# Performance work log

Measured on AMD Instinct MI355X. Metric: run time of the kernel, lower is better.

Reference implementation:

```python
import jax, jax.numpy as jnp
import numpy as np

B, N, C, H = 16, 577, 384, 6
ONE_DIM = 24
RPD = 2 * ONE_DIM - 1  # 47
NUM_CLS = 1
HEAD_DIM = C // H
SCALE = HEAD_DIM ** -0.5


def _build_rel_pos_index():
    # Faithful to the torch loop: tmp[dy - y + off, dx - x + off] with
    # torch's negative-index wraparound -> modulo RPD.
    off = ONE_DIM // 2
    qy = np.repeat(np.arange(ONE_DIM), ONE_DIM)  # (Np,) y of each query patch
    qx = np.tile(np.arange(ONE_DIM), ONE_DIM)    # (Np,) x of each query patch
    ky, kx = qy, qx                              # key patches use same grid
    ry = (ky[None, :] - qy[:, None] + off) % RPD
    rx = (kx[None, :] - qx[:, None] + off) % RPD
    return jnp.asarray(ry * RPD + rx, dtype=jnp.int32)  # (Np, Np)


def setup_inputs() -> dict:
    key = jax.random.key(0)
    k = jax.random.split(key, 6)
    x = jax.random.normal(k[0], (B, N, C), dtype=jnp.float32)
    qkv_w = jax.random.normal(k[1], (3 * C, C), dtype=jnp.float32) * 0.02
    qkv_b = jnp.zeros((3 * C,), dtype=jnp.float32)
    proj_w = jax.random.normal(k[2], (C, C), dtype=jnp.float32) * 0.02
    proj_b = jnp.zeros((C,), dtype=jnp.float32)
    rel_pos = jax.random.normal(k[3], (H, RPD * RPD), dtype=jnp.float32) * 0.02
    mask = jax.random.randint(k[4], (B, N, N), 0, 2, dtype=jnp.int32)
    return {
        "x": x, "qkv_w": qkv_w, "qkv_b": qkv_b,
        "proj_w": proj_w, "proj_b": proj_b, "rel_pos": rel_pos,
        "rel_pos_index": _build_rel_pos_index(),
        "mask": mask, "patch_attn": 1,
    }


def reference(x, qkv_w, qkv_b, proj_w, proj_b, rel_pos, rel_pos_index, mask, patch_attn):
    # qkv projection: torch Linear -> x @ W^T + b
    qkv = x @ qkv_w.T + qkv_b                               # (B, N, 3C)
    qkv = qkv.reshape(B, N, 3, H, HEAD_DIM).transpose(2, 0, 3, 1, 4)
    q, k, v = qkv[0], qkv[1], qkv[2]                        # (B, H, N, hd)

    attn = jnp.einsum("bhqd,bhkd->bhqk", q, k) * SCALE      # (B, H, N, N)

    if patch_attn:
        # gather per-head relative-position bias for patch tokens
        bias = rel_pos[:, rel_pos_index]                    # (H, Np, Np)
        attn = attn.at[:, :, NUM_CLS:, NUM_CLS:].add(bias)

    neg = jnp.finfo(attn.dtype).min
    attn = jnp.where(mask[:, None, :, :] == 0, neg, attn)   # broadcast over heads

    attn = jax.nn.softmax(attn, axis=-1)
    out = jnp.einsum("bhqk,bhkd->bhqd", attn, v)            # (B, H, N, hd)
    out = out.transpose(0, 2, 1, 3).reshape(B, N, C)
    out = out @ proj_w.T + proj_b
    return out
```

## Files before the change

kernel.cpp:

```cpp
#include <hip/hip_runtime.h>
#include <float.h>
#include <math.h>

#define NB 16
#define NN 577
#define NC 384
#define NH 6
#define ND 64
#define RPD2 2209
#define MTOT 9232
#define MPAD 9344
#define SCALE_ 0.125f
#define NEGBIG -3.0e38f
#define BSTRIDE 580
#define NKPAD 640

typedef __attribute__((ext_vector_type(8))) short bf16x8;
typedef __attribute__((ext_vector_type(4))) float f32x4;
typedef unsigned short u16;

#define MFMA16(a, b, c) __builtin_amdgcn_mfma_f32_16x16x32_bf16(a, b, c, 0, 0, 0)

#define SQA 3932160ull
#define OFF_QH 0ull
#define OFF_QL SQA
#define OFF_KH (2ull * SQA)
#define OFF_KL (3ull * SQA)
#define OFF_VTH (4ull * SQA)
#define OFF_VTL (5ull * SQA)
#define OFF_XH (6ull * SQA)
#define OFF_XL (6ull * SQA + 3588096ull)
#define OFF_WQH (6ull * SQA + 2ull * 3588096ull)
#define OFF_WQL (OFF_WQH + 442368ull)
#define OFF_WPH (OFF_WQL + 442368ull)
#define OFF_WPL (OFF_WPH + 147456ull)
#define OFF_BT  (OFF_WPL + 147456ull)
#define OFF_PM  (OFF_BT + 2007960ull)

static __device__ __forceinline__ u16 f2bf(float f) {
  unsigned u = __float_as_uint(f);
  u += 0x7fff + ((u >> 16) & 1);
  return (u16)(u >> 16);
}
static __device__ __forceinline__ float bf2f(u16 h) {
  return __uint_as_float((unsigned)h << 16);
}
static __device__ __forceinline__ void split2(float v, u16& hi, u16& lo) {
  hi = f2bf(v);
  lo = f2bf(v - bf2f(hi));
}
static __device__ __forceinline__ void gload16(const void* g, void* l) {
  __builtin_amdgcn_global_load_lds(
      (const __attribute__((address_space(1))) void*)g,
      (__attribute__((address_space(3))) void*)l, 16, 0, 0);
}

__global__ __launch_bounds__(256) void split_inputs_k(
    const float* __restrict__ x, const float* __restrict__ wq,
    const float* __restrict__ wp, u16* __restrict__ ws)
{
  const int q = blockIdx.x * 256 + threadIdx.x;
  float4 v = {0.f, 0.f, 0.f, 0.f};
  u16 *dh, *dl;
  if (q < 897024) {
    if (q < 886272) v = ((const float4*)x)[q];
    dh = ws + OFF_XH + 4ull * q;
    dl = ws + OFF_XL + 4ull * q;
  } else if (q < 1007616) {
    int t = q - 897024;
    v = ((const float4*)wq)[t];
    dh = ws + OFF_WQH + 4ull * t;
    dl = ws + OFF_WQL + 4ull * t;
  } else {
    int t = q - 1007616;
    v = ((const float4*)wp)[t];
    dh = ws + OFF_WPH + 4ull * t;
    dl = ws + OFF_WPL + 4ull * t;
  }
  ushort4 hh, ll;
  split2(v.x, hh.x, ll.x);
  split2(v.y, hh.y, ll.y);
  split2(v.z, hh.z, ll.z);
  split2(v.w, hh.w, ll.w);
  *(ushort4*)dh = hh;
  *(ushort4*)dl = ll;
}

__global__ __launch_bounds__(256) void pack_mask_k(const int* __restrict__ mask,
                                                   unsigned* __restrict__ pm)
{
  const int wid = (blockIdx.x * 256 + threadIdx.x) >> 6;
  const int lane = threadIdx.x & 63;
  if (wid >= MTOT) return;
  const int* mr = mask + (size_t)wid * NN;
#pragma unroll
  for (int c = 0; c < 10; ++c) {
    int k = c * 64 + lane;
    int v = (k < NN) ? mr[k] : 0;
    unsigned long long bal = __ballot(v != 0);
    if (lane == 0) pm[wid * 20 + 2 * c] = (unsigned)bal;
    if (lane == 1) pm[wid * 20 + 2 * c + 1] = (unsigned)(bal >> 32);
  }
}

__global__ __launch_bounds__(256) void bias_build_k(
    const float* __restrict__ rel_pos, const int* __restrict__ rel_idx,
    const int* __restrict__ patch, u16* __restrict__ tbl)
{
  const int q = blockIdx.x;
  const int h = blockIdx.y;
  const int pa = *patch;
  u16* row = tbl + ((size_t)h * NN + q) * BSTRIDE;
  for (int kk = threadIdx.x; kk < BSTRIDE; kk += 256) {
    float v = 0.f;
    if (pa && q >= 1 && kk >= 1 && kk < NN)
      v = rel_pos[h * RPD2 + rel_idx[(q - 1) * 576 + (kk - 1)]];
    row[kk] = f2bf(v);
  }
}

__global__ __launch_bounds__(256, 3) void qkv_mfma_k(
    const u16* __restrict__ Xh, const u16* __restrict__ Xl,
    const u16* __restrict__ Wh, const u16* __restrict__ Wl,
    const float* __restrict__ bias, u16* __restrict__ ws)
{
  __shared__ u16 Ash[4096], Asl[4096];
  __shared__ u16 Bsh[4096], Bsl[4096];

  const int tid = threadIdx.x;
  const int w = tid >> 6, l = tid & 63, lq = l & 15, lg = l >> 4;
  const int wm = (w >> 1) * 64, wn = (w & 1) * 64;
  const int mb = blockIdx.x * 128;
  const int rb = blockIdx.y * 128;
  const int r0 = rb + wn;
  const int soff = (l >> 2) * 384 + (l & 3) * 8;

  f32x4 acc[4][4];
#pragma unroll
  for (int nt = 0; nt < 4; ++nt) {
    float bv = bias[r0 + 16 * nt + lq];
#pragma unroll
    for (int mt = 0; mt < 4; ++mt) acc[mt][nt] = (f32x4){bv, bv, bv, bv};
  }

  for (int k0 = 0; k0 < 384; k0 += 32) {
    __syncthreads();
#pragma unroll
    for (int j = 0; j < 2; ++j) {
      const int tr = 32 * w + 16 * j;
      const size_t ga = (size_t)(mb + tr) * 384 + k0 + soff;
      const size_t gb = (size_t)(rb + tr) * 384 + k0 + soff;
      gload16(&Xh[ga], &Ash[tr * 32]);
      gload16(&Xl[ga], &Asl[tr * 32]);
      gload16(&Wh[gb], &Bsh[tr * 32]);
      gload16(&Wl[gb], &Bsl[tr * 32]);
    }
    __syncthreads();

    bf16x8 bhf[4], blf[4];
#pragma unroll
    for (int nt = 0; nt < 4; ++nt) {
      bhf[nt] = *(const bf16x8*)&Bsh[(wn + 16 * nt + lq) * 32 + 8 * lg];
      blf[nt] = *(const bf16x8*)&Bsl[(wn + 16 * nt + lq) * 32 + 8 * lg];
    }
#pragma unroll
    for (int mt = 0; mt < 4; ++mt) {
      bf16x8 ah = *(const bf16x8*)&Ash[(wm + 16 * mt + lq) * 32 + 8 * lg];
      bf16x8 al = *(const bf16x8*)&Asl[(wm + 16 * mt + lq) * 32 + 8 * lg];
#pragma unroll
      for (int nt = 0; nt < 4; ++nt) {
        acc[mt][nt] = MFMA16(ah, bhf[nt], acc[mt][nt]);
        acc[mt][nt] = MFMA16(ah, blf[nt], acc[mt][nt]);
        acc[mt][nt] = MFMA16(al, bhf[nt], acc[mt][nt]);
      }
    }
  }

  const int comp = rb / 384;
  const int h = ((rb % 384) + wn) >> 6;
#pragma unroll
  for (int mt = 0; mt < 4; ++mt)
#pragma unroll
    for (int r = 0; r < 4; ++r) {
      int m = mb + wm + 16 * mt + 4 * lg + r;
      if (m >= MTOT) continue;
      int bb = m / NN, nn = m - bb * NN;
      int bh = bb * NH + h;
#pragma unroll
      for (int nt = 0; nt < 4; ++nt) {
        int d = 16 * nt + lq;
        float v = acc[mt][nt][r];
        u16 hi, lo;
        if (comp == 0) {
          v *= SCALE_;
          split2(v, hi, lo);
          size_t a = ((size_t)bh * NKPAD + nn) * 64 + d;
          ws[OFF_QH + a] = hi;
          ws[OFF_QL + a] = lo;
        } else if (comp == 1) {
          split2(v, hi, lo);
          size_t a = ((size_t)bh * NKPAD + nn) * 64 + d;
          ws[OFF_KH + a] = hi;
          ws[OFF_KL + a] = lo;
        } else {
          split2(v, hi, lo);
          size_t a = ((size_t)bh * 64 + d) * NKPAD + nn;
          ws[OFF_VTH + a] = hi;
          ws[OFF_VTL + a] = lo;
        }
      }
    }
}

__global__ __launch_bounds__(256, 3) void attn_k(
    const u16* __restrict__ Qh, const u16* __restrict__ Ql,
    const u16* __restrict__ Kh, const u16* __restrict__ Kl,
    const u16* __restrict__ Vth, const u16* __restrict__ Vtl,
    const u16* __restrict__ btbl, const unsigned* __restrict__ pm,
    u16* __restrict__ Oh, u16* __restrict__ Ol)
{
  __shared__ u16 Kth[4096], Ktl[4096];
  __shared__ u16 Vsh[4096], Vsl[4096];
  __shared__ u16 Ph[4][1024], Pl[4][1024];

  const int tid = threadIdx.x;
  const int w = tid >> 6, l = tid & 63, lq = l & 15, lg = l >> 4;
  const int q0 = blockIdx.x * 64;
  const int h = blockIdx.y, b = blockIdx.z;
  const int bh = b * NH + h;
  const int qrow = q0 + 16 * w + lq;
  const int swz = (lq & 7) << 3;
  const int ln8 = l >> 3, lc8 = l & 7;
  const int koff = ln8 * 64 + ((lc8 ^ ln8) << 3);
  const int voff = ln8 * NKPAD + ((lc8 ^ ln8) << 3);

  const size_t qbase = ((size_t)bh * NKPAD + qrow) * 64 + 8 * lg;
  bf16x8 qbh[2], qbl[2];
  qbh[0] = *(const bf16x8*)&Qh[qbase];
  qbh[1] = *(const bf16x8*)&Qh[qbase + 32];
  qbl[0] = *(const bf16x8*)&Ql[qbase];
  qbl[1] = *(const bf16x8*)&Ql[qbase + 32];

  const bool qv = qrow < NN;
  const int gqc = qv ? qrow : NN - 1;
  const unsigned* pmrow = pm + ((size_t)b * NN + gqc) * 20;
  const size_t brow = ((size_t)h * NN + gqc) * BSTRIDE;

  float m_reg = NEGBIG, l_reg = 0.f;
  f32x4 accO[4] = {};

  for (int ch = 0; ch < 10; ++ch) {
    const int kb = ch * 64;
    __syncthreads();
    {
      const size_t kgb = ((size_t)bh * NKPAD + kb + 16 * w) * 64 + koff;
      const size_t vgb = ((size_t)bh * 64 + 16 * w) * NKPAD + kb + voff;
      gload16(&Kh[kgb],                 &Kth[(16 * w) * 64]);
      gload16(&Kh[kgb + 512],           &Kth[(16 * w + 8) * 64]);
      gload16(&Kl[kgb],                 &Ktl[(16 * w) * 64]);
      gload16(&Kl[kgb + 512],           &Ktl[(16 * w + 8) * 64]);
      gload16(&Vth[vgb],                &Vsh[(16 * w) * 64]);
      gload16(&Vth[vgb + 8 * NKPAD],    &Vsh[(16 * w + 8) * 64]);
      gload16(&Vtl[vgb],                &Vsl[(16 * w) * 64]);
      gload16(&Vtl[vgb + 8 * NKPAD],    &Vsl[(16 * w + 8) * 64]);
    }
    unsigned long long m64 = (unsigned long long)pmrow[2 * ch] |
                             ((unsigned long long)pmrow[2 * ch + 1] << 32);
    f32x4 cinit[4];
#pragma unroll
    for (int t = 0; t < 4; ++t) {
      cinit[t] = (f32x4){0.f, 0.f, 0.f, 0.f};
      int kkb = kb + 16 * t + 4 * lg;
      if (qv && kkb <= 576) {
        ushort4 b4 = *(const ushort4*)&btbl[brow + kkb];
        cinit[t][0] = bf2f(b4.x); cinit[t][1] = bf2f(b4.y);
        cinit[t][2] = bf2f(b4.z); cinit[t][3] = bf2f(b4.w);
      }
    }
    __syncthreads();

    float sv[4][4];
#pragma unroll
    for (int t = 0; t < 4; ++t) {
      f32x4 acc = cinit[t];
      const int ar = (16 * t + lq) * 64;
#pragma unroll
      for (int ks = 0; ks < 2; ++ks) {
        const int c = (8 * lg + 32 * ks) ^ swz;
        bf16x8 ah = *(const bf16x8*)&Kth[ar + c];
        bf16x8 al = *(const bf16x8*)&Ktl[ar + c];
        acc = MFMA16(ah, qbh[ks], acc);
        acc = MFMA16(ah, qbl[ks], acc);
        acc = MFMA16(al, qbh[ks], acc);
      }
      sv[t][0] = acc[0]; sv[t][1] = acc[1];
      sv[t][2] = acc[2]; sv[t][3] = acc[3];
    }

    float cmax = NEGBIG;
#pragma unroll
    for (int t = 0; t < 4; ++t)
#pragma unroll
      for (int r = 0; r < 4; ++r) {
        int kl = 16 * t + 4 * lg + r;
        float s = ((m64 >> kl) & 1ull) ? sv[t][r] : NEGBIG;
        sv[t][r] = s;
        cmax = fmaxf(cmax, s);
      }
    cmax = fmaxf(cmax, __shfl_xor(cmax, 16));
    cmax = fmaxf(cmax, __shfl_xor(cmax, 32));
    float m_new = fmaxf(m_reg, cmax);
    float fx = __expf(m_reg - m_new);
    float csum = 0.f;
    float ev[4][4];
#pragma unroll
    for (int t = 0; t < 4; ++t)
#pragma unroll
      for (int r = 0; r < 4; ++r) {
        float e = __expf(sv[t][r] - m_new);
        ev[t][r] = e;
        csum += e;
      }
    csum += __shfl_xor(csum, 16);
    csum += __shfl_xor(csum, 32);
    l_reg = l_reg * fx + csum;
    m_reg = m_new;

#pragma unroll
    for (int t = 0; t < 4; ++t) {
      ushort4 ph, plo;
      split2(ev[t][0], ph.x, plo.x);
      split2(ev[t][1], ph.y, plo.y);
      split2(ev[t][2], ph.z, plo.z);
      split2(ev[t][3], ph.w, plo.w);
      int c = (16 * t + 4 * lg) ^ swz;
      *(ushort4*)&Ph[w][lq * 64 + c] = ph;
      *(ushort4*)&Pl[w][lq * 64 + c] = plo;
    }

    float fxr[4];
#pragma unroll
    for (int r = 0; r < 4; ++r) fxr[r] = __shfl(fx, 4 * lg + r);
#pragma unroll
    for (int t = 0; t < 4; ++t) {
      accO[t][0] *= fxr[0]; accO[t][1] *= fxr[1];
      accO[t][2] *= fxr[2]; accO[t][3] *= fxr[3];
    }

    bf16x8 pah[2], pal[2];
#pragma unroll
    for (int ks = 0; ks < 2; ++ks) {
      int c = (8 * lg + 32 * ks) ^ swz;
      pah[ks] = *(const bf16x8*)&Ph[w][lq * 64 + c];
      pal[ks] = *(const bf16x8*)&Pl[w][lq * 64 + c];
    }

#pragma unroll
    for (int t = 0; t < 4; ++t) {
      const int vr = (16 * t + lq) * 64;
#pragma unroll
      for (int ks = 0; ks < 2; ++ks) {
        const int c = (8 * lg + 32 * ks) ^ swz;
        bf16x8 vh = *(const bf16x8*)&Vsh[vr + c];
        bf16x8 vl = *(const bf16x8*)&Vsl[vr + c];
        accO[t] = MFMA16(pah[ks], vh, accO[t]);
        accO[t] = MFMA16(pal[ks], vh, accO[t]);
        accO[t] = MFMA16(pah[ks], vl, accO[t]);
      }
    }
  }

  float il = 1.f / l_reg;
  float ilr[4];
#pragma unroll
  for (int r = 0; r < 4; ++r) ilr[r] = __shfl(il, 4 * lg + r);
#pragma unroll
  for (int t = 0; t < 4; ++t)
#pragma unroll
    for (int r = 0; r < 4; ++r) {
      int gq2 = q0 + 16 * w + 4 * lg + r;
      if (gq2 < NN) {
        float v = accO[t][r] * ilr[r];
        u16 hi, lo;
        split2(v, hi, lo);
        size_t a = ((size_t)b * NN + gq2) * NC + h * 64 + 16 * t + lq;
        Oh[a] = hi;
        Ol[a] = lo;
      }
    }
}

__global__ __launch_bounds__(256, 3) void proj_mfma_k(
    const u16* __restrict__ Ah, const u16* __restrict__ Al,
    const u16* __restrict__ Wh, const u16* __restrict__ Wl,
    const float* __restrict__ bias, float* __restrict__ out)
{
  __shared__ u16 Ash[4096], Asl[4096];
  __shared__ u16 Bsh[4096], Bsl[4096];

  const int tid = threadIdx.x;
  const int w = tid >> 6, l = tid & 63, lq = l & 15, lg = l >> 4;
  const int wm = (w >> 1) * 64, wn = (w & 1) * 64;
  const int mb = blockIdx.x * 128;
  const int rb = blockIdx.y * 128;
  const int r0 = rb + wn;
  const int soff = (l >> 2) * 384 + (l & 3) * 8;

  f32x4 acc[4][4];
#pragma unroll
  for (int nt = 0; nt < 4; ++nt) {
    float bv = bias[r0 + 16 * nt + lq];
#pragma unroll
    for (int mt = 0; mt < 4; ++mt) acc[mt][nt] = (f32x4){bv, bv, bv, bv};
  }

  for (int k0 = 0; k0 < 384; k0 += 32) {
    __syncthreads();
#pragma unroll
    for (int j = 0; j < 2; ++j) {
      const int tr = 32 * w + 16 * j;
      const size_t ga = (size_t)(mb + tr) * 384 + k0 + soff;
      const size_t gb = (size_t)(rb + tr) * 384 + k0 + soff;
      gload16(&Ah[ga], &Ash[tr * 32]);
      gload16(&Al[ga], &Asl[tr * 32]);
      gload16(&Wh[gb], &Bsh[tr * 32]);
      gload16(&Wl[gb], &Bsl[tr * 32]);
    }
    __syncthreads();

    bf16x8 bhf[4], blf[4];
#pragma unroll
    for (int nt = 0; nt < 4; ++nt) {
      bhf[nt] = *(const bf16x8*)&Bsh[(wn + 16 * nt + lq) * 32 + 8 * lg];
      blf[nt] = *(const bf16x8*)&Bsl[(wn + 16 * nt + lq) * 32 + 8 * lg];
    }
#pragma unroll
    for (int mt = 0; mt < 4; ++mt) {
      bf16x8 ah = *(const bf16x8*)&Ash[(wm + 16 * mt + lq) * 32 + 8 * lg];
      bf16x8 al = *(const bf16x8*)&Asl[(wm + 16 * mt + lq) * 32 + 8 * lg];
#pragma unroll
      for (int nt = 0; nt < 4; ++nt) {
        acc[mt][nt] = MFMA16(ah, bhf[nt], acc[mt][nt]);
        acc[mt][nt] = MFMA16(ah, blf[nt], acc[mt][nt]);
        acc[mt][nt] = MFMA16(al, bhf[nt], acc[mt][nt]);
      }
    }
  }

#pragma unroll
  for (int mt = 0; mt < 4; ++mt)
#pragma unroll
    for (int r = 0; r < 4; ++r) {
      int m = mb + wm + 16 * mt + 4 * lg + r;
      if (m >= MTOT) continue;
#pragma unroll
      for (int nt = 0; nt < 4; ++nt)
        out[(size_t)m * NC + r0 + 16 * nt + lq] = acc[mt][nt][r];
    }
}

extern "C" void kernel_launch(void* const* d_in, const int* in_sizes, int n_in,
                              void* d_out, int out_size, void* d_ws, size_t ws_size,
                              hipStream_t stream) {
  const float* x       = (const float*)d_in[0];
  const float* qkv_w   = (const float*)d_in[1];
  const float* qkv_b   = (const float*)d_in[2];
  const float* proj_w  = (const float*)d_in[3];
  const float* proj_b  = (const float*)d_in[4];
  const float* rel_pos = (const float*)d_in[5];
  const int*   rel_idx = (const int*)d_in[6];
  const int*   mask    = (const int*)d_in[7];
  const int*   patch   = (const int*)d_in[8];
  float* out = (float*)d_out;
  u16* W16 = (u16*)d_ws;

  unsigned* pmp = (unsigned*)(W16 + OFF_PM);
  u16* btblp = W16 + OFF_BT;

  split_inputs_k<<<4080, 256, 0, stream>>>(x, qkv_w, proj_w, W16);
  pack_mask_k<<<2308, 256, 0, stream>>>(mask, pmp);
  bias_build_k<<<dim3(NN, NH), 256, 0, stream>>>(rel_pos, rel_idx, patch, btblp);
  qkv_mfma_k<<<dim3(73, 9), 256, 0, stream>>>(
      W16 + OFF_XH, W16 + OFF_XL, W16 + OFF_WQH, W16 + OFF_WQL, qkv_b, W16);
  attn_k<<<dim3(10, NH, NB), 256, 0, stream>>>(
      W16 + OFF_QH, W16 + OFF_QL, W16 + OFF_KH, W16 + OFF_KL,
      W16 + OFF_VTH, W16 + OFF_VTL, btblp, pmp,
      W16 + OFF_XH, W16 + OFF_XL);
  proj_mfma_k<<<dim3(73, 3), 256, 0, stream>>>(
      W16 + OFF_XH, W16 + OFF_XL, W16 + OFF_WPH, W16 + OFF_WPL, proj_b, out);
}
```

Measured before the change: 181.5 us.

## Rewrite attention kernel with 32x32 MFMA, 128-query tiles and XCD-aware block mapping

Switches the attention kernel from 16x16x32 to 32x32x16 bf16 MFMA, with each wave owning 32 query rows so a block covers 128 queries. K/V LDS tiles are reused across twice as many queries, halving block count and global K/V traffic. The P matrix is now kept as a single bf16 (dropping the lo term in PV, 2 MFMAs instead of 3), which reduces work but lowers precision of the softmax weights. Blocks are remapped so the same (b,h) lands on the same XCD for L2 locality.

```diff
diff --git a/kernel.cpp b/kernel.cpp
--- a/kernel.cpp
+++ b/kernel.cpp
@@ -17,9 +17,11 @@
 
 typedef __attribute__((ext_vector_type(8))) short bf16x8;
 typedef __attribute__((ext_vector_type(4))) float f32x4;
+typedef __attribute__((ext_vector_type(16))) float f32x16;
 typedef unsigned short u16;
 
 #define MFMA16(a, b, c) __builtin_amdgcn_mfma_f32_16x16x32_bf16(a, b, c, 0, 0, 0)
+#define MFMA32(a, b, c) __builtin_amdgcn_mfma_f32_32x32x16_bf16(a, b, c, 0, 0, 0)
 
 #define SQA 3932160ull
 #define OFF_QH 0ull
@@ -221,33 +223,39 @@
 {
   __shared__ u16 Kth[4096], Ktl[4096];
   __shared__ u16 Vsh[4096], Vsl[4096];
-  __shared__ u16 Ph[4][1024], Pl[4][1024];
+  __shared__ u16 Ps[4][2048];
 
   const int tid = threadIdx.x;
-  const int w = tid >> 6, l = tid & 63, lq = l & 15, lg = l >> 4;
-  const int q0 = blockIdx.x * 64;
-  const int h = blockIdx.y, b = blockIdx.z;
-  const int bh = b * NH + h;
-  const int qrow = q0 + 16 * w + lq;
-  const int swz = (lq & 7) << 3;
+  const int w = tid >> 6, l = tid & 63;
+  const int qc = l & 31, hi = l >> 5;
+
+  const int wg = blockIdx.x;
+  const int xcd = wg & 7, slot = wg >> 3;
+  const int bh = (slot / 5) * 8 + xcd;
+  const int qb = slot % 5;
+  const int b = bh / NH, h = bh % NH;
+  const int q0 = qb * 128;
+
+  const int q = q0 + 32 * w + qc;
   const int ln8 = l >> 3, lc8 = l & 7;
   const int koff = ln8 * 64 + ((lc8 ^ ln8) << 3);
   const int voff = ln8 * NKPAD + ((lc8 ^ ln8) << 3);
 
-  const size_t qbase = ((size_t)bh * NKPAD + qrow) * 64 + 8 * lg;
-  bf16x8 qbh[2], qbl[2];
-  qbh[0] = *(const bf16x8*)&Qh[qbase];
-  qbh[1] = *(const bf16x8*)&Qh[qbase + 32];
-  qbl[0] = *(const bf16x8*)&Ql[qbase];
-  qbl[1] = *(const bf16x8*)&Ql[qbase + 32];
-
-  const bool qv = qrow < NN;
-  const int gqc = qv ? qrow : NN - 1;
-  const unsigned* pmrow = pm + ((size_t)b * NN + gqc) * 20;
-  const size_t brow = ((size_t)h * NN + gqc) * BSTRIDE;
+  const size_t qrow = ((size_t)bh * NKPAD + q) * 64 + 8 * hi;
+  bf16x8 qfh[4], qfl[4];
+#pragma unroll
+  for (int st = 0; st < 4; ++st) {
+    qfh[st] = *(const bf16x8*)&Qh[qrow + 16 * st];
+    qfl[st] = *(const bf16x8*)&Ql[qrow + 16 * st];
+  }
+
+  const bool qv = q < NN;
+  const int gq = qv ? q : NN - 1;
+  const unsigned* pmrow = pm + ((size_t)b * NN + gq) * 20;
+  const size_t brow = ((size_t)h * NN + gq) * BSTRIDE;
 
   float m_reg = NEGBIG, l_reg = 0.f;
-  f32x4 accO[4] = {};
+  f32x16 accO[2] = {};
 
   for (int ch = 0; ch < 10; ++ch) {
     const int kb = ch * 64;
@@ -255,137 +263,131 @@
     {
       const size_t kgb = ((size_t)bh * NKPAD + kb + 16 * w) * 64 + koff;
       const size_t vgb = ((size_t)bh * 64 + 16 * w) * NKPAD + kb + voff;
-      gload16(&Kh[kgb],                 &Kth[(16 * w) * 64]);
-      gload16(&Kh[kgb + 512],           &Kth[(16 * w + 8) * 64]);
-      gload16(&Kl[kgb],                 &Ktl[(16 * w) * 64]);
-      gload16(&Kl[kgb + 512],           &Ktl[(16 * w + 8) * 64]);
-      gload16(&Vth[vgb],                &Vsh[(16 * w) * 64]);
-      gload16(&Vth[vgb + 8 * NKPAD],    &Vsh[(16 * w + 8) * 64]);
-      gload16(&Vtl[vgb],                &Vsl[(16 * w) * 64]);
-      gload16(&Vtl[vgb + 8 * NKPAD],    &Vsl[(16 * w + 8) * 64]);
+      gload16(&Kh[kgb],              &Kth[(16 * w) * 64]);
+      gload16(&Kh[kgb + 512],        &Kth[(16 * w + 8) * 64]);
+      gload16(&Kl[kgb],              &Ktl[(16 * w) * 64]);
+      gload16(&Kl[kgb + 512],        &Ktl[(16 * w + 8) * 64]);
+      gload16(&Vth[vgb],             &Vsh[(16 * w) * 64]);
+      gload16(&Vth[vgb + 8 * NKPAD], &Vsh[(16 * w + 8) * 64]);
+      gload16(&Vtl[vgb],             &Vsl[(16 * w) * 64]);
+      gload16(&Vtl[vgb + 8 * NKPAD], &Vsl[(16 * w + 8) * 64]);
     }
     unsigned long long m64 = (unsigned long long)pmrow[2 * ch] |
                              ((unsigned long long)pmrow[2 * ch + 1] << 32);
-    f32x4 cinit[4];
-#pragma unroll
-    for (int t = 0; t < 4; ++t) {
-      cinit[t] = (f32x4){0.f, 0.f, 0.f, 0.f};
-      int kkb = kb + 16 * t + 4 * lg;
-      if (qv && kkb <= 576) {
-        ushort4 b4 = *(const ushort4*)&btbl[brow + kkb];
-        cinit[t][0] = bf2f(b4.x); cinit[t][1] = bf2f(b4.y);
-        cinit[t][2] = bf2f(b4.z); cinit[t][3] = bf2f(b4.w);
-      }
-    }
-    __syncthreads();
-
-    float sv[4][4];
-#pragma unroll
-    for (int t = 0; t < 4; ++t) {
-      f32x4 acc = cinit[t];
-      const int ar = (16 * t + lq) * 64;
-#pragma unroll
-      for (int ks = 0; ks < 2; ++ks) {
-        const int c = (8 * lg + 32 * ks) ^ swz;
-        bf16x8 ah = *(const bf16x8*)&Kth[ar + c];
-        bf16x8 al = *(const bf16x8*)&Ktl[ar + c];
-        acc = MFMA16(ah, qbh[ks], acc);
-        acc = MFMA16(ah, qbl[ks], acc);
-        acc = MFMA16(al, qbh[ks], acc);
-      }
-      sv[t][0] = acc[0]; sv[t][1] = acc[1];
-      sv[t][2] = acc[2]; sv[t][3] = acc[3];
+    f32x16 s[2];
+#pragma unroll
+    for (int kt = 0; kt < 2; ++kt) {
+#pragma unroll
+      for (int m = 0; m < 4; ++m) {
+        int kkb = kb + 32 * kt + 8 * m + 4 * hi;
+        ushort4 b4 = {0, 0, 0, 0};
+        if (qv && kkb <= 576) b4 = *(const ushort4*)&btbl[brow + kkb];
+        s[kt][4 * m + 0] = bf2f(b4.x);
+        s[kt][4 * m + 1] = bf2f(b4.y);
+        s[kt][4 * m + 2] = bf2f(b4.z);
+        s[kt][4 * m + 3] = bf2f(b4.w);
+      }
+    }
+    __syncthreads();
+
+#pragma unroll
+    for (int kt = 0; kt < 2; ++kt) {
+      const int key = 32 * kt + qc;
+      const int rbase = key * 64;
+      const int sw = (key & 7);
+#pragma unroll
+      for (int st = 0; st < 4; ++st) {
+        const int addr = rbase + (((2 * st + hi) ^ sw) << 3);
+        bf16x8 ah = *(const bf16x8*)&Kth[addr];
+        bf16x8 al = *(const bf16x8*)&Ktl[addr];
+        s[kt] = MFMA32(ah, qfh[st], s[kt]);
+        s[kt] = MFMA32(ah, qfl[st], s[kt]);
+        s[kt] = MFMA32(al, qfh[st], s[kt]);
+      }
     }
 
     float cmax = NEGBIG;
 #pragma unroll
-    for (int t = 0; t < 4; ++t)
-#pragma unroll
-      for (int r = 0; r < 4; ++r) {
-        int kl = 16 * t + 4 * lg + r;
-        float s = ((m64 >> kl) & 1ull) ? sv[t][r] : NEGBIG;
-        sv[t][r] = s;
-        cmax = fmaxf(cmax, s);
-      }
-    cmax = fmaxf(cmax, __shfl_xor(cmax, 16));
+    for (int kt = 0; kt < 2; ++kt)
+#pragma unroll
+      for (int r = 0; r < 16; ++r) {
+        int bit = 32 * kt + (r & 3) + 8 * (r >> 2) + 4 * hi;
+        float v = ((m64 >> bit) & 1ull) ? s[kt][r] : NEGBIG;
+        s[kt][r] = v;
+        cmax = fmaxf(cmax, v);
+      }
     cmax = fmaxf(cmax, __shfl_xor(cmax, 32));
     float m_new = fmaxf(m_reg, cmax);
     float fx = __expf(m_reg - m_new);
     float csum = 0.f;
-    float ev[4][4];
-#pragma unroll
-    for (int t = 0; t < 4; ++t)
-#pragma unroll
-      for (int r = 0; r < 4; ++r) {
-        float e = __expf(sv[t][r] - m_new);
-        ev[t][r] = e;
-        csum += e;
-      }
-    csum += __shfl_xor(csum, 16);
+#pragma unroll
+    for (int kt = 0; kt < 2; ++kt)
+#pragma unroll
+      for (int m = 0; m < 4; ++m) {
+        ushort4 pk;
+        float e0 = __expf(s[kt][4 * m + 0] - m_new);
+        float e1 = __expf(s[kt][4 * m + 1] - m_new);
+        float e2 = __expf(s[kt][4 * m + 2] - m_new);
+        float e3 = __expf(s[kt][4 * m + 3] - m_new);
+        csum += e0 + e1 + e2 + e3;
+        pk.x = f2bf(e0); pk.y = f2bf(e1); pk.z = f2bf(e2); pk.w = f2bf(e3);
+        int saddr = qc * 64 + (((4 * kt + m) ^ (qc & 7)) << 3) + 4 * hi;
+        *(ushort4*)&Ps[w][saddr] = pk;
+      }
     csum += __shfl_xor(csum, 32);
     l_reg = l_reg * fx + csum;
     m_reg = m_new;
 
 #pragma unroll
-    for (int t = 0; t < 4; ++t) {
-      ushort4 ph, plo;
-      split2(ev[t][0], ph.x, plo.x);
-      split2(ev[t][1], ph.y, plo.y);
-      split2(ev[t][2], ph.z, plo.z);
-      split2(ev[t][3], ph.w, plo.w);
-      int c = (16 * t + 4 * lg) ^ swz;
-      *(ushort4*)&Ph[w][lq * 64 + c] = ph;
-      *(ushort4*)&Pl[w][lq * 64 + c] = plo;
-    }
-
-    float fxr[4];
-#pragma unroll
-    for (int r = 0; r < 4; ++r) fxr[r] = __shfl(fx, 4 * lg + r);
-#pragma unroll
-    for (int t = 0; t < 4; ++t) {
-      accO[t][0] *= fxr[0]; accO[t][1] *= fxr[1];
-      accO[t][2] *= fxr[2]; accO[t][3] *= fxr[3];
-    }
-
-    bf16x8 pah[2], pal[2];
-#pragma unroll
-    for (int ks = 0; ks < 2; ++ks) {
-      int c = (8 * lg + 32 * ks) ^ swz;
-      pah[ks] = *(const bf16x8*)&Ph[w][lq * 64 + c];
-      pal[ks] = *(const bf16x8*)&Pl[w][lq * 64 + c];
-    }
-
-#pragma unroll
-    for (int t = 0; t < 4; ++t) {
-      const int vr = (16 * t + lq) * 64;
-#pragma unroll
-      for (int ks = 0; ks < 2; ++ks) {
-        const int c = (8 * lg + 32 * ks) ^ swz;
-        bf16x8 vh = *(const bf16x8*)&Vsh[vr + c];
-        bf16x8 vl = *(const bf16x8*)&Vsl[vr + c];
-        accO[t] = MFMA16(pah[ks], vh, accO[t]);
-        accO[t] = MFMA16(pal[ks], vh, accO[t]);
-        accO[t] = MFMA16(pah[ks], vl, accO[t]);
+    for (int r = 0; r < 16; ++r) {
+      int qr = (r & 3) + 8 * (r >> 2) + 4 * hi;
+      float fxr = __shfl(fx, 32 * w + qr);
+      accO[0][r] *= fxr;
+      accO[1][r] *= fxr;
+    }
+
+    bf16x8 pa[4];
+#pragma unroll
+    for (int st = 0; st < 4; ++st) {
+      int addr = qc * 64 + (((2 * st + hi) ^ (qc & 7)) << 3);
+      pa[st] = *(const bf16x8*)&Ps[w][addr];
+    }
+
+#pragma unroll
+    for (int dt = 0; dt < 2; ++dt) {
+      const int d = 32 * dt + qc;
+      const int rbase = d * 64;
+      const int sw = (d & 7);
+#pragma unroll
+      for (int st = 0; st < 4; ++st) {
+        const int addr = rbase + (((2 * st + hi) ^ sw) << 3);
+        bf16x8 vh = *(const bf16x8*)&Vsh[addr];
+        bf16x8 vl = *(const bf16x8*)&Vsl[addr];
+        accO[dt] = MFMA32(pa[st], vh, accO[dt]);
+        accO[dt] = MFMA32(pa[st], vl, accO[dt]);
       }
     }
   }
 
   float il = 1.f / l_reg;
-  float ilr[4];
-#pragma unroll
-  for (int r = 0; r < 4; ++r) ilr[r] = __shfl(il, 4 * lg + r);
-#pragma unroll
-  for (int t = 0; t < 4; ++t)
-#pragma unroll
-    for (int r = 0; r < 4; ++r) {
-      int gq2 = q0 + 16 * w + 4 * lg + r;
+  float ilr[16];
+#pragma unroll
+  for (int r = 0; r < 16; ++r) {
+    int qr = (r & 3) + 8 * (r >> 2) + 4 * hi;
+    ilr[r] = __shfl(il, 32 * w + qr);
+  }
+#pragma unroll
+  for (int dt = 0; dt < 2; ++dt)
+#pragma unroll
+    for (int r = 0; r < 16; ++r) {
+      int gq2 = q0 + 32 * w + (r & 3) + 8 * (r >> 2) + 4 * hi;
       if (gq2 < NN) {
-        float v = accO[t][r] * ilr[r];
-        u16 hi, lo;
-        split2(v, hi, lo);
-        size_t a = ((size_t)b * NN + gq2) * NC + h * 64 + 16 * t + lq;
-        Oh[a] = hi;
-        Ol[a] = lo;
+        float v = accO[dt][r] * ilr[r];
+        u16 vh_, vl_;
+        split2(v, vh_, vl_);
+        size_t a = ((size_t)b * NN + gq2) * NC + h * 64 + 32 * dt + qc;
+        Oh[a] = vh_;
+        Ol[a] = vl_;
       }
     }
 }
@@ -482,7 +484,7 @@
   bias_build_k<<<dim3(NN, NH), 256, 0, stream>>>(rel_pos, rel_idx, patch, btblp);
   qkv_mfma_k<<<dim3(73, 9), 256, 0, stream>>>(
       W16 + OFF_XH, W16 + OFF_XL, W16 + OFF_WQH, W16 + OFF_WQL, qkv_b, W16);
-  attn_k<<<dim3(10, NH, NB), 256, 0, stream>>>(
+  attn_k<<<480, 256, 0, stream>>>(
       W16 + OFF_QH, W16 + OFF_QL, W16 + OFF_KH, W16 + OFF_KL,
       W16 + OFF_VTH, W16 + OFF_VTL, btblp, pmp,
       W16 + OFF_XH, W16 + OFF_XL);
```

Result: slower. 255.0 us (+40.5%).

## Double-buffer K/V tiles in attention and drop low half of P

Applied to the files above, without the earlier changes.

Gives the attention kernel's K and V shared-memory tiles two buffers. The next 64-key chunk is prefetched while the current one is being computed, which removes the second barrier in each iteration. It also stops splitting the softmax probabilities P into a bf16 high/low pair: P is kept only as bf16, which removes one MFMA per PV step and the Pl shared buffer. The larger LDS footprint lowers the launch bound from 3 to 2 blocks per CU, and P now carries less precision than before.

```diff
diff --git a/kernel.cpp b/kernel.cpp
--- a/kernel.cpp
+++ b/kernel.cpp
@@ -212,16 +212,16 @@
     }
 }
 
-__global__ __launch_bounds__(256, 3) void attn_k(
+__global__ __launch_bounds__(256, 2) void attn_k(
     const u16* __restrict__ Qh, const u16* __restrict__ Ql,
     const u16* __restrict__ Kh, const u16* __restrict__ Kl,
     const u16* __restrict__ Vth, const u16* __restrict__ Vtl,
     const u16* __restrict__ btbl, const unsigned* __restrict__ pm,
     u16* __restrict__ Oh, u16* __restrict__ Ol)
 {
-  __shared__ u16 Kth[4096], Ktl[4096];
-  __shared__ u16 Vsh[4096], Vsl[4096];
-  __shared__ u16 Ph[4][1024], Pl[4][1024];
+  __shared__ u16 Kth[2][4096], Ktl[2][4096];
+  __shared__ u16 Vsh[2][4096], Vsl[2][4096];
+  __shared__ u16 Ph[4][1024];
 
   const int tid = threadIdx.x;
   const int w = tid >> 6, l = tid & 63, lq = l & 15, lg = l >> 4;
@@ -234,6 +234,23 @@
   const int koff = ln8 * 64 + ((lc8 ^ ln8) << 3);
   const int voff = ln8 * NKPAD + ((lc8 ^ ln8) << 3);
 
+#define STAGE(ch, bf)                                                        \
+  {                                                                          \
+    const int kb_ = (ch) * 64;                                               \
+    const size_t kgb = ((size_t)bh * NKPAD + kb_ + 16 * w) * 64 + koff;      \
+    const size_t vgb = ((size_t)bh * 64 + 16 * w) * NKPAD + kb_ + voff;      \
+    gload16(&Kh[kgb],              &Kth[bf][(16 * w) * 64]);                 \
+    gload16(&Kh[kgb + 512],        &Kth[bf][(16 * w + 8) * 64]);             \
+    gload16(&Kl[kgb],              &Ktl[bf][(16 * w) * 64]);                 \
+    gload16(&Kl[kgb + 512],        &Ktl[bf][(16 * w + 8) * 64]);             \
+    gload16(&Vth[vgb],             &Vsh[bf][(16 * w) * 64]);                 \
+    gload16(&Vth[vgb + 8 * NKPAD], &Vsh[bf][(16 * w + 8) * 64]);             \
+    gload16(&Vtl[vgb],             &Vsl[bf][(16 * w) * 64]);                 \
+    gload16(&Vtl[vgb + 8 * NKPAD], &Vsl[bf][(16 * w + 8) * 64]);             \
+  }
+
+  STAGE(0, 0);
+
   const size_t qbase = ((size_t)bh * NKPAD + qrow) * 64 + 8 * lg;
   bf16x8 qbh[2], qbl[2];
   qbh[0] = *(const bf16x8*)&Qh[qbase];
@@ -251,19 +268,10 @@
 
   for (int ch = 0; ch < 10; ++ch) {
     const int kb = ch * 64;
+    const int bf = ch & 1;
     __syncthreads();
-    {
-      const size_t kgb = ((size_t)bh * NKPAD + kb + 16 * w) * 64 + koff;
-      const size_t vgb = ((size_t)bh * 64 + 16 * w) * NKPAD + kb + voff;
-      gload16(&Kh[kgb],                 &Kth[(16 * w) * 64]);
-      gload16(&Kh[kgb + 512],           &Kth[(16 * w + 8) * 64]);
-      gload16(&Kl[kgb],                 &Ktl[(16 * w) * 64]);
-      gload16(&Kl[kgb + 512],           &Ktl[(16 * w + 8) * 64]);
-      gload16(&Vth[vgb],                &Vsh[(16 * w) * 64]);
-      gload16(&Vth[vgb + 8 * NKPAD],    &Vsh[(16 * w + 8) * 64]);
-      gload16(&Vtl[vgb],                &Vsl[(16 * w) * 64]);
-      gload16(&Vtl[vgb + 8 * NKPAD],    &Vsl[(16 * w + 8) * 64]);
-    }
+    if (ch < 9) STAGE(ch + 1, bf ^ 1);
+
     unsigned long long m64 = (unsigned long long)pmrow[2 * ch] |
                              ((unsigned long long)pmrow[2 * ch + 1] << 32);
     f32x4 cinit[4];
@@ -277,7 +285,6 @@
         cinit[t][2] = bf2f(b4.z); cinit[t][3] = bf2f(b4.w);
       }
     }
-    __syncthreads();
 
     float sv[4][4];
 #pragma unroll
@@ -287,8 +294,8 @@
 #pragma unroll
       for (int ks = 0; ks < 2; ++ks) {
         const int c = (8 * lg + 32 * ks) ^ swz;
-        bf16x8 ah = *(const bf16x8*)&Kth[ar + c];
-        bf16x8 al = *(const bf16x8*)&Ktl[ar + c];
+        bf16x8 ah = *(const bf16x8*)&Kth[bf][ar + c];
+        bf16x8 al = *(const bf16x8*)&Ktl[bf][ar + c];
         acc = MFMA16(ah, qbh[ks], acc);
         acc = MFMA16(ah, qbl[ks], acc);
         acc = MFMA16(al, qbh[ks], acc);
@@ -328,14 +335,13 @@
 
 #pragma unroll
     for (int t = 0; t < 4; ++t) {
-      ushort4 ph, plo;
-      split2(ev[t][0], ph.x, plo.x);
-      split2(ev[t][1], ph.y, plo.y);
-      split2(ev[t][2], ph.z, plo.z);
-      split2(ev[t][3], ph.w, plo.w);
+      ushort4 ph;
+      ph.x = f2bf(ev[t][0]);
+      ph.y = f2bf(ev[t][1]);
+      ph.z = f2bf(ev[t][2]);
+      ph.w = f2bf(ev[t][3]);
       int c = (16 * t + 4 * lg) ^ swz;
       *(ushort4*)&Ph[w][lq * 64 + c] = ph;
-      *(ushort4*)&Pl[w][lq * 64 + c] = plo;
     }
 
     float fxr[4];
@@ -347,12 +353,11 @@
       accO[t][2] *= fxr[2]; accO[t][3] *= fxr[3];
     }
 
-    bf16x8 pah[2], pal[2];
+    bf16x8 pah[2];
 #pragma unroll
     for (int ks = 0; ks < 2; ++ks) {
       int c = (8 * lg + 32 * ks) ^ swz;
       pah[ks] = *(const bf16x8*)&Ph[w][lq * 64 + c];
-      pal[ks] = *(const bf16x8*)&Pl[w][lq * 64 + c];
     }
 
 #pragma unroll
@@ -361,10 +366,9 @@
 #pragma unroll
       for (int ks = 0; ks < 2; ++ks) {
         const int c = (8 * lg + 32 * ks) ^ swz;
-        bf16x8 vh = *(const bf16x8*)&Vsh[vr + c];
-        bf16x8 vl = *(const bf16x8*)&Vsl[vr + c];
+        bf16x8 vh = *(const bf16x8*)&Vsh[bf][vr + c];
+        bf16x8 vl = *(const bf16x8*)&Vsl[bf][vr + c];
         accO[t] = MFMA16(pah[ks], vh, accO[t]);
-        accO[t] = MFMA16(pal[ks], vh, accO[t]);
         accO[t] = MFMA16(pah[ks], vl, accO[t]);
       }
     }
@@ -388,6 +392,7 @@
         Ol[a] = lo;
       }
     }
+#undef STAGE
 }
 
 __global__ __launch_bounds__(256, 3) void proj_mfma_k(
```

Measured after the change: 171.2 us. -5.7%, faster.
